# Kernel optimization log

Hardware: AMD Instinct MI355X
Metric: run time of the kernel (lower is better)

## Reference

```python
import jax, jax.numpy as jnp
import numpy as np

N = 100000
E = 3200000
F_IN = 512
HID = 16
N_CLS = 40


def setup_inputs() -> dict:
    key = jax.random.key(0)
    k1, k2, k3, k4, k5, k6 = jax.random.split(key, 6)
    x = jax.random.normal(k1, (N, F_IN), dtype=jnp.float32)
    edge_index = jax.random.randint(k2, (2, E), 0, N, dtype=jnp.int64)
    # Glorot-ish init for layer weights (as in PyG GCNConv defaults)
    W1 = jax.random.normal(k3, (F_IN, HID), dtype=jnp.float32) * (1.0 / np.sqrt(F_IN))
    b1 = jnp.zeros((HID,), dtype=jnp.float32)
    W2 = jax.random.normal(k4, (HID, N_CLS), dtype=jnp.float32) * (1.0 / np.sqrt(HID))
    b2 = jnp.zeros((N_CLS,), dtype=jnp.float32)
    return {"x": x, "W1": W1, "b1": b1, "W2": W2, "b2": b2, "edge_index": edge_index}


def _gcn_norm(edge_index, n):
    # Add self-loops, compute symmetric normalization deg^{-1/2} (A+I) deg^{-1/2}
    loops = jnp.arange(n, dtype=edge_index.dtype)
    src = jnp.concatenate([edge_index[0], loops])  # [E+N]
    dst = jnp.concatenate([edge_index[1], loops])  # [E+N]
    ones = jnp.ones(src.shape, dtype=jnp.float32)
    deg = jax.ops.segment_sum(ones, dst, num_segments=n)  # in-degree with self-loops
    dinv = jnp.where(deg > 0, jax.lax.rsqrt(deg), 0.0)
    norm = dinv[src] * dinv[dst]  # [E+N]
    return src, dst, norm


def _gcn_conv(h, W, b, src, dst, norm, n):
    h = h @ W  # transform first (cheaper: small out dim)
    msg = h[src] * norm[:, None]           # gather + scale
    out = jax.ops.segment_sum(msg, dst, num_segments=n)  # scatter-add
    return out + b


def reference(x, W1, b1, W2, b2, edge_index):
    n = x.shape[0]
    src, dst, norm = _gcn_norm(edge_index, n)
    h = _gcn_conv(x, W1, b1, src, dst, norm, n)
    h = jax.nn.relu(h)
    # F.dropout(training=self.training): identity in eval mode
    h = _gcn_conv(h, W2, b2, src, dst, norm, n)
    return jax.nn.log_softmax(h, axis=1)
```

## Files before the change

kernel.cpp:

```cpp
#include <hip/hip_runtime.h>

typedef __attribute__((ext_vector_type(8))) short short8;
typedef __attribute__((ext_vector_type(4))) float floatx4;

#define CHUNK 8192
#define SHIFT 8
#define CAP   12288

__device__ __forceinline__ short f2bf(float f) {
    unsigned int u = __float_as_uint(f);
    u = (u + 0x7FFFu + ((u >> 16) & 1u)) >> 16;
    return (short)u;
}


__global__ __launch_bounds__(256) void blockhist(const int* __restrict__ dst, int* __restrict__ ghist,
                                                 int E, int nbuk, int nblk) {
    __shared__ int lh[512];
    int tid = threadIdx.x, blk = blockIdx.x;
    for (int i = tid; i < nbuk; i += 256) lh[i] = 0;
    __syncthreads();
    int base = blk * CHUNK;
    int end = base + CHUNK; if (end > E) end = E;
    for (int i = base + tid; i < end; i += 256)
        atomicAdd(&lh[dst[i] >> SHIFT], 1);
    __syncthreads();
    for (int i = tid; i < nbuk; i += 256) ghist[(size_t)i * nblk + blk] = lh[i];
}

__global__ __launch_bounds__(512) void rowscan(int* __restrict__ ghist, int* __restrict__ btot,
                                               int nbuk, int nblk) {
    __shared__ int s[512];
    int k = blockIdx.x, tid = threadIdx.x;
    int v = (tid < nblk) ? ghist[(size_t)k * nblk + tid] : 0;
    s[tid] = v; __syncthreads();
    for (int d = 1; d < 512; d <<= 1) {
        int t = (tid >= d) ? s[tid - d] : 0;
        __syncthreads();
        s[tid] += t;
        __syncthreads();
    }
    if (tid < nblk) ghist[(size_t)k * nblk + tid] = k * CAP + (s[tid] - v);
    if (tid == nblk - 1) btot[k] = s[tid];
}

__global__ __launch_bounds__(256) void binpass(const int* __restrict__ eidx, const int* __restrict__ ghist,
                                               unsigned* __restrict__ ebin, int E, int nbuk, int nblk) {
    __shared__ int lh[512];
    __shared__ int lb[512];
    __shared__ int lim[512];
    int tid = threadIdx.x, blk = blockIdx.x;
    for (int i = tid; i < nbuk; i += 256) {
        int b = ghist[(size_t)i * nblk + blk];
        lh[i] = 0; lb[i] = b; lim[i] = (i + 1) * CAP - b;
    }
    __syncthreads();
    int base = blk * CHUNK;
    int end = base + CHUNK; if (end > E) end = E;
    for (int i = base + tid; i < end; i += 256) {
        unsigned s = (unsigned)eidx[i];
        unsigned d = (unsigned)eidx[E + i];
        int buk = d >> SHIFT;
        int r = atomicAdd(&lh[buk], 1);
        if (r < lim[buk])
            ebin[lb[buk] + r] = s | ((d & 255u) << 24);
    }
}

__global__ __launch_bounds__(256) void permB(const int* __restrict__ btot,
                                             int* __restrict__ off, int* __restrict__ cnt,
                                             float* __restrict__ dinv,
                                             unsigned* __restrict__ ebin,
                                             int N) {
    __shared__ unsigned stage[CAP];
    __shared__ int hist[256];
    __shared__ int sc[256];
    __shared__ int obase[256];
    __shared__ int lcur[256];
    int k = blockIdx.x, tid = threadIdx.x;
    int n0 = k << SHIFT;
    int bstart = k * CAP;
    int cntb = btot[k]; if (cntb > CAP) cntb = CAP;
    hist[tid] = 0;
    __syncthreads();
    for (int i = tid; i < cntb; i += 256) {
        unsigned p = ebin[bstart + i];
        stage[i] = p;
        atomicAdd(&hist[p >> 24], 1);
    }
    __syncthreads();
    int h = hist[tid];
    sc[tid] = h; __syncthreads();
    for (int d = 1; d < 256; d <<= 1) {
        int t = (tid >= d) ? sc[tid - d] : 0;
        __syncthreads();
        sc[tid] += t;
        __syncthreads();
    }
    int excl = sc[tid] - h;
    int nn = n0 + tid;
    if (nn < N) {
        off[nn] = bstart + excl;
        cnt[nn] = h;
        dinv[nn] = rsqrtf((float)(h + 1));
    }
    obase[tid] = bstart + excl;
    lcur[tid] = 0;
    __syncthreads();
    for (int i = tid; i < cntb; i += 256) {
        unsigned p = stage[i];
        int d = p >> 24;
        int r = atomicAdd(&lcur[d], 1);
        ebin[obase[d] + r] = p & 0xFFFFFFu;
    }
}

__global__ __launch_bounds__(256) void gemm1_mfma(const float* __restrict__ x,
                                                  const float* __restrict__ w1,
                                                  const float* __restrict__ dinv,
                                                  float* __restrict__ g1,
                                                  int ntiles, int N) {
    __shared__ __align__(16) float wl[512 * 16];
    int tid = threadIdx.x;
    for (int i = tid; i < 2048; i += 256)
        ((float4*)wl)[i] = ((const float4*)w1)[i];
    __syncthreads();

    int lane = tid & 63;
    int q = lane >> 4, r = lane & 15;

    short8 bf[16];
#pragma unroll
    for (int kk = 0; kk < 16; ++kk) {
        int kb = kk * 32 + q * 8;
        short8 t;
#pragma unroll
        for (int j = 0; j < 8; ++j) t[j] = f2bf(wl[(kb + j) * 16 + r]);
        bf[kk] = t;
    }

    int tile = blockIdx.x * 4 + (tid >> 6);
    if (tile >= ntiles) return;
    int nb = tile * 16;
    int row = nb + r; if (row >= N) row = N - 1;
    const float* xp = x + (size_t)row * 512 + q * 8;
    floatx4 acc = {0.f, 0.f, 0.f, 0.f};
#pragma unroll
    for (int kk = 0; kk < 16; ++kk) {
        float4 a0 = *(const float4*)(xp + kk * 32);
        float4 a1 = *(const float4*)(xp + kk * 32 + 4);
        short8 af;
        af[0] = f2bf(a0.x); af[1] = f2bf(a0.y); af[2] = f2bf(a0.z); af[3] = f2bf(a0.w);
        af[4] = f2bf(a1.x); af[5] = f2bf(a1.y); af[6] = f2bf(a1.z); af[7] = f2bf(a1.w);
        acc = __builtin_amdgcn_mfma_f32_16x16x32_bf16(af, bf[kk], acc, 0, 0, 0);
    }
#pragma unroll
    for (int i = 0; i < 4; ++i) {
        int rr = nb + q * 4 + i;
        if (rr < N) g1[(size_t)rr * 16 + r] = acc[i] * dinv[rr];
    }
}

__device__ __forceinline__ float4 shfl_xor4(float4 v, int d) {
    float4 r;
    r.x = __shfl_xor(v.x, d, 64);
    r.y = __shfl_xor(v.y, d, 64);
    r.z = __shfl_xor(v.z, d, 64);
    r.w = __shfl_xor(v.w, d, 64);
    return r;
}
__device__ __forceinline__ float4 add4(float4 a, float4 b) {
    return make_float4(a.x + b.x, a.y + b.y, a.z + b.z, a.w + b.w);
}

__global__ __launch_bounds__(256) void agg16w(const float* __restrict__ in, float* __restrict__ out,
                                              const int* __restrict__ off, const int* __restrict__ cnt,
                                              const float* __restrict__ dinv,
                                              const unsigned* __restrict__ edges,
                                              const float* __restrict__ bias, int N) {
    int t = blockIdx.x * blockDim.x + threadIdx.x;
    int n = t >> 6;
    if (n >= N) return;
    int lane = t & 63;
    int h4 = lane & 3, j = lane >> 2;
    int p0 = off[n], c = cnt[n];
    const unsigned* ep = edges + p0;
    float4 acc = make_float4(0.f, 0.f, 0.f, 0.f);
    for (int i = j; i < c; i += 32) {
        int i2 = i + 16;
        unsigned sa = ep[i];
        unsigned sb = (i2 < c) ? ep[i2] : 0u;
        acc = add4(acc, *(const float4*)(in + (size_t)sa * 16 + h4 * 4));
        if (i2 < c) acc = add4(acc, *(const float4*)(in + (size_t)sb * 16 + h4 * 4));
    }
#pragma unroll
    for (int d = 4; d < 64; d <<= 1) acc = add4(acc, shfl_xor4(acc, d));
    if (j == 0) {
        float di = dinv[n];
        float4 sv = *(const float4*)(in + (size_t)n * 16 + h4 * 4);
        float4 b4 = *(const float4*)(bias + h4 * 4);
        float4 v;
        v.x = fmaxf(di * (acc.x + sv.x) + b4.x, 0.f) * di;
        v.y = fmaxf(di * (acc.y + sv.y) + b4.y, 0.f) * di;
        v.z = fmaxf(di * (acc.z + sv.z) + b4.z, 0.f) * di;
        v.w = fmaxf(di * (acc.w + sv.w) + b4.w, 0.f) * di;
        *(float4*)(out + (size_t)n * 16 + h4 * 4) = v;
    }
}

__global__ __launch_bounds__(256) void agg_out(const float* __restrict__ in,
                                               const int* __restrict__ off, const int* __restrict__ cnt,
                                               const float* __restrict__ dinv,
                                               const unsigned* __restrict__ edges,
                                               const float* __restrict__ w2,
                                               const float* __restrict__ b2,
                                               float* __restrict__ out, int N) {
    __shared__ float w2s[704];
    __shared__ float b2s[40];
    int tid = threadIdx.x;
    for (int i = tid; i < 704; i += 256) w2s[i] = (i < 640) ? w2[i] : 0.0f;
    if (tid < 40) b2s[tid] = b2[tid];
    __syncthreads();

    int n = blockIdx.x * 4 + (tid >> 6);
    if (n >= N) return;
    int lane = tid & 63;
    int h4 = lane & 3, j = lane >> 2;
    int p0 = off[n], c = cnt[n];
    const unsigned* ep = edges + p0;
    float4 acc = make_float4(0.f, 0.f, 0.f, 0.f);
    for (int i = j; i < c; i += 32) {
        int i2 = i + 16;
        unsigned sa = ep[i];
        unsigned sb = (i2 < c) ? ep[i2] : 0u;
        acc = add4(acc, *(const float4*)(in + (size_t)sa * 16 + h4 * 4));
        if (i2 < c) acc = add4(acc, *(const float4*)(in + (size_t)sb * 16 + h4 * 4));
    }
#pragma unroll
    for (int d = 4; d < 64; d <<= 1) acc = add4(acc, shfl_xor4(acc, d));
    float di = dinv[n];
    float4 sv = *(const float4*)(in + (size_t)n * 16 + h4 * 4);
    float4 v4;
    v4.x = di * (acc.x + sv.x);
    v4.y = di * (acc.y + sv.y);
    v4.z = di * (acc.z + sv.z);
    v4.w = di * (acc.w + sv.w);

    float a2k[16];
#pragma unroll
    for (int k = 0; k < 16; ++k) {
        float comp = (k & 3) == 0 ? v4.x : (k & 3) == 1 ? v4.y : (k & 3) == 2 ? v4.z : v4.w;
        a2k[k] = __shfl(comp, k >> 2, 64);
    }

    bool act = lane < 40;
    float dot = act ? b2s[lane] : 0.0f;
#pragma unroll
    for (int k = 0; k < 16; ++k)
        dot += a2k[k] * w2s[k * 40 + lane];

    float v = act ? dot : -__builtin_inff();
#pragma unroll
    for (int s = 32; s > 0; s >>= 1) v = fmaxf(v, __shfl_xor(v, s, 64));
    float ex = act ? expf(dot - v) : 0.0f;
    float ssum = ex;
#pragma unroll
    for (int s = 32; s > 0; s >>= 1) ssum += __shfl_xor(ssum, s, 64);
    float lse = logf(ssum);
    if (act) out[(size_t)n * 40 + lane] = dot - v - lse;
}


extern "C" void kernel_launch(void* const* d_in, const int* in_sizes, int n_in,
                              void* d_out, int out_size, void* d_ws, size_t ws_size,
                              hipStream_t stream) {
    const float* x   = (const float*)d_in[0];
    const float* W1  = (const float*)d_in[1];
    const float* b1  = (const float*)d_in[2];
    const float* W2  = (const float*)d_in[3];
    const float* b2  = (const float*)d_in[4];
    const int*   eidx = (const int*)d_in[5];
    float* out = (float*)d_out;

    const int N = in_sizes[0] / 512;
    const int E = in_sizes[5] / 2;

    const int NBUK = (N + 255) >> SHIFT;
    const int nblk = (E + CHUNK - 1) / CHUNK;
    const int M = NBUK * nblk;

    char* w = (char*)d_ws;
    auto alloc = [&](size_t bytes) { char* p = w; w += (bytes + 255) & ~(size_t)255; return p; };
    int*      off   = (int*)alloc((size_t)N * 4);
    int*      cnt   = (int*)alloc((size_t)N * 4);
    float*    dinv  = (float*)alloc((size_t)N * 4);
    int*      btot  = (int*)alloc((size_t)NBUK * 4);
    int*      ghist = (int*)alloc((size_t)M * 4);
    unsigned* ebin  = (unsigned*)alloc((size_t)NBUK * CAP * 4);
    float*    g1    = (float*)alloc((size_t)N * 16 * 4);
    float*    r1    = (float*)alloc((size_t)N * 16 * 4);
    float*    a2    = g1;

    blockhist<<<nblk, 256, 0, stream>>>(eidx + E, ghist, E, NBUK, nblk);
    rowscan<<<NBUK, 512, 0, stream>>>(ghist, btot, NBUK, nblk);
    binpass<<<nblk, 256, 0, stream>>>(eidx, ghist, ebin, E, NBUK, nblk);
    permB<<<NBUK, 256, 0, stream>>>(btot, off, cnt, dinv, ebin, N);

    int ntiles = (N + 15) / 16;
    gemm1_mfma<<<(ntiles + 3) / 4, 256, 0, stream>>>(x, W1, dinv, g1, ntiles, N);

    agg16w<<<((size_t)N * 64 + 255) / 256, 256, 0, stream>>>(g1, r1, off, cnt, dinv, ebin, b1, N);
    agg_out<<<(N + 3) / 4, 256, 0, stream>>>(r1, off, cnt, dinv, ebin, W2, b2, out, N);
    (void)a2;
}
```

Baseline: 526.9 us.

## Use nontemporal streaming loads, 4-tile GEMM per wave, deeper gather unroll

Streaming reads of the edge index, the x matrix and the edge lists now use nontemporal loads so they do less harm to cache residency of the gathered feature rows. The first-layer GEMM makes each wave process four 16-row tiles, which reuses the register-held bf16 W1 fragments and issues more loads per wave, with a quarter as many blocks. Both aggregation kernels gather four neighbours per iteration instead of two to raise memory-level parallelism. The costs are higher register pressure and fewer waves in the GEMM.

```diff
diff --git a/kernel.cpp b/kernel.cpp
--- a/kernel.cpp
+++ b/kernel.cpp
@@ -23,7 +23,7 @@
     int base = blk * CHUNK;
     int end = base + CHUNK; if (end > E) end = E;
     for (int i = base + tid; i < end; i += 256)
-        atomicAdd(&lh[dst[i] >> SHIFT], 1);
+        atomicAdd(&lh[__builtin_nontemporal_load(&dst[i]) >> SHIFT], 1);
     __syncthreads();
     for (int i = tid; i < nbuk; i += 256) ghist[(size_t)i * nblk + blk] = lh[i];
 }
@@ -58,8 +58,8 @@
     int base = blk * CHUNK;
     int end = base + CHUNK; if (end > E) end = E;
     for (int i = base + tid; i < end; i += 256) {
-        unsigned s = (unsigned)eidx[i];
-        unsigned d = (unsigned)eidx[E + i];
+        unsigned s = (unsigned)__builtin_nontemporal_load(&eidx[i]);
+        unsigned d = (unsigned)__builtin_nontemporal_load(&eidx[E + i]);
         int buk = d >> SHIFT;
         int r = atomicAdd(&lh[buk], 1);
         if (r < lim[buk])
@@ -119,7 +119,7 @@
                                                   const float* __restrict__ w1,
                                                   const float* __restrict__ dinv,
                                                   float* __restrict__ g1,
-                                                  int ntiles, int N) {
+                                                  int N) {
     __shared__ __align__(16) float wl[512 * 16];
     int tid = threadIdx.x;
     for (int i = tid; i < 2048; i += 256)
@@ -139,25 +139,42 @@
         bf[kk] = t;
     }
 
-    int tile = blockIdx.x * 4 + (tid >> 6);
-    if (tile >= ntiles) return;
-    int nb = tile * 16;
-    int row = nb + r; if (row >= N) row = N - 1;
-    const float* xp = x + (size_t)row * 512 + q * 8;
-    floatx4 acc = {0.f, 0.f, 0.f, 0.f};
+    int rowbase = blockIdx.x * 256 + (tid >> 6) * 64;
+    if (rowbase >= N) return;
+
+    const float* xp[4];
+#pragma unroll
+    for (int t = 0; t < 4; ++t) {
+        int row = rowbase + t * 16 + r; if (row >= N) row = N - 1;
+        xp[t] = x + (size_t)row * 512 + q * 8;
+    }
+    floatx4 acc[4];
+#pragma unroll
+    for (int t = 0; t < 4; ++t) acc[t] = (floatx4){0.f, 0.f, 0.f, 0.f};
+
 #pragma unroll
     for (int kk = 0; kk < 16; ++kk) {
-        float4 a0 = *(const float4*)(xp + kk * 32);
-        float4 a1 = *(const float4*)(xp + kk * 32 + 4);
-        short8 af;
-        af[0] = f2bf(a0.x); af[1] = f2bf(a0.y); af[2] = f2bf(a0.z); af[3] = f2bf(a0.w);
-        af[4] = f2bf(a1.x); af[5] = f2bf(a1.y); af[6] = f2bf(a1.z); af[7] = f2bf(a1.w);
-        acc = __builtin_amdgcn_mfma_f32_16x16x32_bf16(af, bf[kk], acc, 0, 0, 0);
-    }
-#pragma unroll
-    for (int i = 0; i < 4; ++i) {
-        int rr = nb + q * 4 + i;
-        if (rr < N) g1[(size_t)rr * 16 + r] = acc[i] * dinv[rr];
+        floatx4 a0[4], a1[4];
+#pragma unroll
+        for (int t = 0; t < 4; ++t) {
+            a0[t] = __builtin_nontemporal_load((const floatx4*)(xp[t] + kk * 32));
+            a1[t] = __builtin_nontemporal_load((const floatx4*)(xp[t] + kk * 32 + 4));
+        }
+#pragma unroll
+        for (int t = 0; t < 4; ++t) {
+            short8 af;
+            af[0] = f2bf(a0[t][0]); af[1] = f2bf(a0[t][1]); af[2] = f2bf(a0[t][2]); af[3] = f2bf(a0[t][3]);
+            af[4] = f2bf(a1[t][0]); af[5] = f2bf(a1[t][1]); af[6] = f2bf(a1[t][2]); af[7] = f2bf(a1[t][3]);
+            acc[t] = __builtin_amdgcn_mfma_f32_16x16x32_bf16(af, bf[kk], acc[t], 0, 0, 0);
+        }
+    }
+#pragma unroll
+    for (int t = 0; t < 4; ++t) {
+#pragma unroll
+        for (int i = 0; i < 4; ++i) {
+            int rr = rowbase + t * 16 + q * 4 + i;
+            if (rr < N) g1[(size_t)rr * 16 + r] = acc[t][i] * dinv[rr];
+        }
     }
 }
 
@@ -186,12 +203,20 @@
     int p0 = off[n], c = cnt[n];
     const unsigned* ep = edges + p0;
     float4 acc = make_float4(0.f, 0.f, 0.f, 0.f);
-    for (int i = j; i < c; i += 32) {
-        int i2 = i + 16;
-        unsigned sa = ep[i];
-        unsigned sb = (i2 < c) ? ep[i2] : 0u;
-        acc = add4(acc, *(const float4*)(in + (size_t)sa * 16 + h4 * 4));
-        if (i2 < c) acc = add4(acc, *(const float4*)(in + (size_t)sb * 16 + h4 * 4));
+    for (int i = j; i < c; i += 64) {
+        int i1 = i + 16, i2 = i + 32, i3 = i + 48;
+        unsigned s0 = __builtin_nontemporal_load(&ep[i]);
+        unsigned s1 = 0u, s2 = 0u, s3 = 0u;
+        if (i1 < c) s1 = __builtin_nontemporal_load(&ep[i1]);
+        if (i2 < c) s2 = __builtin_nontemporal_load(&ep[i2]);
+        if (i3 < c) s3 = __builtin_nontemporal_load(&ep[i3]);
+        float4 v0 = *(const float4*)(in + (size_t)s0 * 16 + h4 * 4);
+        float4 v1 = make_float4(0.f, 0.f, 0.f, 0.f);
+        float4 v2 = v1, v3 = v1;
+        if (i1 < c) v1 = *(const float4*)(in + (size_t)s1 * 16 + h4 * 4);
+        if (i2 < c) v2 = *(const float4*)(in + (size_t)s2 * 16 + h4 * 4);
+        if (i3 < c) v3 = *(const float4*)(in + (size_t)s3 * 16 + h4 * 4);
+        acc = add4(acc, add4(add4(v0, v1), add4(v2, v3)));
     }
 #pragma unroll
     for (int d = 4; d < 64; d <<= 1) acc = add4(acc, shfl_xor4(acc, d));
@@ -229,12 +254,20 @@
     int p0 = off[n], c = cnt[n];
     const unsigned* ep = edges + p0;
     float4 acc = make_float4(0.f, 0.f, 0.f, 0.f);
-    for (int i = j; i < c; i += 32) {
-        int i2 = i + 16;
-        unsigned sa = ep[i];
-        unsigned sb = (i2 < c) ? ep[i2] : 0u;
-        acc = add4(acc, *(const float4*)(in + (size_t)sa * 16 + h4 * 4));
-        if (i2 < c) acc = add4(acc, *(const float4*)(in + (size_t)sb * 16 + h4 * 4));
+    for (int i = j; i < c; i += 64) {
+        int i1 = i + 16, i2 = i + 32, i3 = i + 48;
+        unsigned s0 = __builtin_nontemporal_load(&ep[i]);
+        unsigned s1 = 0u, s2 = 0u, s3 = 0u;
+        if (i1 < c) s1 = __builtin_nontemporal_load(&ep[i1]);
+        if (i2 < c) s2 = __builtin_nontemporal_load(&ep[i2]);
+        if (i3 < c) s3 = __builtin_nontemporal_load(&ep[i3]);
+        float4 v0 = *(const float4*)(in + (size_t)s0 * 16 + h4 * 4);
+        float4 v1 = make_float4(0.f, 0.f, 0.f, 0.f);
+        float4 v2 = v1, v3 = v1;
+        if (i1 < c) v1 = *(const float4*)(in + (size_t)s1 * 16 + h4 * 4);
+        if (i2 < c) v2 = *(const float4*)(in + (size_t)s2 * 16 + h4 * 4);
+        if (i3 < c) v3 = *(const float4*)(in + (size_t)s3 * 16 + h4 * 4);
+        acc = add4(acc, add4(add4(v0, v1), add4(v2, v3)));
     }
 #pragma unroll
     for (int d = 4; d < 64; d <<= 1) acc = add4(acc, shfl_xor4(acc, d));
@@ -299,17 +332,14 @@
     unsigned* ebin  = (unsigned*)alloc((size_t)NBUK * CAP * 4);
     float*    g1    = (float*)alloc((size_t)N * 16 * 4);
     float*    r1    = (float*)alloc((size_t)N * 16 * 4);
-    float*    a2    = g1;
 
     blockhist<<<nblk, 256, 0, stream>>>(eidx + E, ghist, E, NBUK, nblk);
     rowscan<<<NBUK, 512, 0, stream>>>(ghist, btot, NBUK, nblk);
     binpass<<<nblk, 256, 0, stream>>>(eidx, ghist, ebin, E, NBUK, nblk);
     permB<<<NBUK, 256, 0, stream>>>(btot, off, cnt, dinv, ebin, N);
 
-    int ntiles = (N + 15) / 16;
-    gemm1_mfma<<<(ntiles + 3) / 4, 256, 0, stream>>>(x, W1, dinv, g1, ntiles, N);
+    gemm1_mfma<<<(N + 255) / 256, 256, 0, stream>>>(x, W1, dinv, g1, N);
 
     agg16w<<<((size_t)N * 64 + 255) / 256, 256, 0, stream>>>(g1, r1, off, cnt, dinv, ebin, b1, N);
     agg_out<<<(N + 3) / 4, 256, 0, stream>>>(r1, off, cnt, dinv, ebin, W2, b2, out, N);
-    (void)a2;
-}
+}
```

Measured after the change: 523.5 us. Within noise of the previous version (-0.6%).
